# Kernel tuning notes

Measured on AMD Instinct MI355X. Metric: run time of the kernel, lower is better.

Reference implementation:

```python
import jax, jax.numpy as jnp
import numpy as np

B, C, N = 16, 256, 2048
D = C // 8  # q/k channel dim = 32
EPS = 1e-5
NEG_SLOPE = 0.2


def _conv1x1(x, w, b):
    # x: [B,C,N], w: [O,C], b: [O] -> [B,O,N]
    return jnp.einsum('oc,bcn->bon', w, x) + b[None, :, None]


def _bn(y, gamma, beta):
    # BatchNorm1d training-mode: per-channel stats over (batch, length)
    m = y.mean(axis=(0, 2), keepdims=True)
    v = y.var(axis=(0, 2), keepdims=True)  # biased, matches torch normalization
    return (y - m) * jax.lax.rsqrt(v + EPS) * gamma[None, :, None] + beta[None, :, None]


def setup_inputs() -> dict:
    key = jax.random.key(0)
    ks = jax.random.split(key, 14)
    s_qk = 1.0 / np.sqrt(C)
    return {
        'x': jax.random.normal(ks[0], (B, C, N), dtype=jnp.float32),
        'q_w': jax.random.normal(ks[1], (D, C), dtype=jnp.float32) * s_qk,
        'q_b': jnp.zeros((D,), jnp.float32),
        'q_g': jnp.ones((D,), jnp.float32),
        'q_be': jnp.zeros((D,), jnp.float32),
        'k_w': jax.random.normal(ks[2], (D, C), dtype=jnp.float32) * s_qk,
        'k_b': jnp.zeros((D,), jnp.float32),
        'k_g': jnp.ones((D,), jnp.float32),
        'k_be': jnp.zeros((D,), jnp.float32),
        'v_w': jax.random.normal(ks[3], (C, C), dtype=jnp.float32) * s_qk,
        'v_b': jnp.zeros((C,), jnp.float32),
        'v_g': jnp.ones((C,), jnp.float32),
        'v_be': jnp.zeros((C,), jnp.float32),
    }


def reference(x, q_w, q_b, q_g, q_be, k_w, k_b, k_g, k_be, v_w, v_b, v_g, v_be):
    # q, k: conv1x1 -> BN (no activation); v: conv1x1 -> BN -> LeakyReLU(0.2)
    q = _bn(_conv1x1(x, q_w, q_b), q_g, q_be)          # [B,D,N]
    k = _bn(_conv1x1(x, k_w, k_b), k_g, k_be)          # [B,D,N]
    v = jax.nn.leaky_relu(_bn(_conv1x1(x, v_w, v_b), v_g, v_be), NEG_SLOPE)  # [B,C,N]
    energy = jnp.einsum('bdn,bdm->bnm', q, k)          # [B,N,N]
    attn = jax.nn.softmax(energy, axis=-1)
    o = jnp.einsum('bcm,bnm->bcn', v, attn)            # attn applied over points
    return o + x
```

## Files before the change

kernel.cpp:

```cpp
#include <hip/hip_runtime.h>

#define BATCH 16
#define CH    256
#define NPT   2048
#define DQK   32
#define OTOT  320
#define EPSB  1e-5f
#define SLOPE 0.2f

typedef __attribute__((ext_vector_type(8))) short bf16x8;
typedef __attribute__((ext_vector_type(4))) float f32x4;

__device__ __forceinline__ unsigned short f2bf(float f) {
    unsigned u = __float_as_uint(f);
    u = (u + 0x7FFFu + ((u >> 16) & 1u)) >> 16;
    return (unsigned short)u;
}
__device__ __forceinline__ float bf2f(unsigned short h) {
    return __uint_as_float(((unsigned)h) << 16);
}
__device__ __forceinline__ unsigned cvt_pk_bf16(float a, float b) {
    unsigned r;
    asm("v_cvt_pk_bf16_f32 %0, %1, %2" : "=v"(r) : "v"(a), "v"(b));
    return r;
}

__global__ __launch_bounds__(256) void prep_kernel(
    const float* __restrict__ qw, const float* __restrict__ qb,
    const float* __restrict__ kw, const float* __restrict__ kb,
    const float* __restrict__ vw, const float* __restrict__ vb,
    unsigned short* __restrict__ Whi, unsigned short* __restrict__ Wlo,
    float* __restrict__ Bv)
{
    int idx = blockIdx.x * 256 + threadIdx.x;
    int o = idx >> 8, c = idx & 255;
    float w;
    if (o < 32)      w = qw[(size_t)o * CH + c];
    else if (o < 64) w = kw[(size_t)(o - 32) * CH + c];
    else             w = vw[(size_t)(o - 64) * CH + c];
    unsigned short wh = f2bf(w);
    float rem = w - bf2f(wh);
    Whi[idx] = wh;
    Wlo[idx] = f2bf(rem);
    if (idx < OTOT) {
        int oo = idx;
        float bb;
        if (oo < 32)      bb = qb[oo];
        else if (oo < 64) bb = kb[oo - 32];
        else              bb = vb[oo - 64];
        Bv[oo] = bb;
    }
}

__global__ __launch_bounds__(256) void conv_kernel(
    const float* __restrict__ x,
    const unsigned short* __restrict__ Whi, const unsigned short* __restrict__ Wlo,
    const float* __restrict__ Bv,
    unsigned short* __restrict__ Ybf,
    float* __restrict__ Sum, float* __restrict__ Sq)
{
    int lin = blockIdx.x;
    int vid = (lin & 7) * 160 + (lin >> 3);
    int o5  = vid % 5;
    int rem = vid / 5;
    int ob = o5 * 64;
    int n0 = (rem & 15) * 128;
    int b  = rem >> 4;

    int tid = threadIdx.x;
    int w = tid >> 6, lane = tid & 63;
    int quad = lane >> 4, l16 = lane & 15;
    int wo = w >> 1, wn = w & 1;

    __shared__ unsigned short Xh[128][40];
    __shared__ unsigned short Xl[128][40];

    int nl = tid & 127;
    int ch = tid >> 7;
    const float* xb = x + (size_t)b * CH * NPT + n0 + nl;

    f32x4 acc[2][4];
#pragma unroll
    for (int ot = 0; ot < 2; ++ot)
#pragma unroll
        for (int nt = 0; nt < 4; ++nt)
            acc[ot][nt] = (f32x4){0.f, 0.f, 0.f, 0.f};

    float xv[16];
#pragma unroll
    for (int i = 0; i < 16; ++i)
        xv[i] = xb[(size_t)(ch * 16 + i) * NPT];

    for (int ks = 0; ks < 8; ++ks) {
        __syncthreads();
#pragma unroll
        for (int g = 0; g < 4; ++g) {
            ushort4 h4, l4;
            unsigned short* ph = (unsigned short*)&h4;
            unsigned short* pl = (unsigned short*)&l4;
#pragma unroll
            for (int j = 0; j < 4; ++j) {
                float f = xv[g * 4 + j];
                unsigned short h = f2bf(f);
                ph[j] = h;
                pl[j] = f2bf(f - bf2f(h));
            }
            *(ushort4*)&Xh[nl][ch * 16 + g * 4] = h4;
            *(ushort4*)&Xl[nl][ch * 16 + g * 4] = l4;
        }
        __syncthreads();

        if (ks < 7) {
#pragma unroll
            for (int i = 0; i < 16; ++i)
                xv[i] = xb[(size_t)((ks + 1) * 32 + ch * 16 + i) * NPT];
        }

        bf16x8 ah[2], al[2];
#pragma unroll
        for (int ot = 0; ot < 2; ++ot) {
            size_t orow = (size_t)(ob + wo * 32 + ot * 16 + l16) * 256 + ks * 32 + quad * 8;
            ah[ot] = *(const bf16x8*)(Whi + orow);
            al[ot] = *(const bf16x8*)(Wlo + orow);
        }
#pragma unroll
        for (int nt = 0; nt < 4; ++nt) {
            int nr = wn * 64 + nt * 16 + l16;
            bf16x8 bh = *(const bf16x8*)&Xh[nr][quad * 8];
            bf16x8 bl = *(const bf16x8*)&Xl[nr][quad * 8];
#pragma unroll
            for (int ot = 0; ot < 2; ++ot) {
                acc[ot][nt] = __builtin_amdgcn_mfma_f32_16x16x32_bf16(ah[ot], bh, acc[ot][nt], 0, 0, 0);
                acc[ot][nt] = __builtin_amdgcn_mfma_f32_16x16x32_bf16(ah[ot], bl, acc[ot][nt], 0, 0, 0);
                acc[ot][nt] = __builtin_amdgcn_mfma_f32_16x16x32_bf16(al[ot], bh, acc[ot][nt], 0, 0, 0);
            }
        }
    }

#pragma unroll
    for (int ot = 0; ot < 2; ++ot) {
        int obase = ob + wo * 32 + ot * 16 + quad * 4;
        float bias[4], sv[4], sq[4];
#pragma unroll
        for (int r = 0; r < 4; ++r) {
            bias[r] = Bv[obase + r];
            sv[r] = 0.f; sq[r] = 0.f;
        }
#pragma unroll
        for (int nt = 0; nt < 4; ++nt) {
            int n = n0 + wn * 64 + nt * 16 + l16;
#pragma unroll
            for (int r = 0; r < 4; ++r) {
                float v = acc[ot][nt][r] + bias[r];
                Ybf[((size_t)b * OTOT + obase + r) * NPT + n] = f2bf(v);
                sv[r] += v; sq[r] += v * v;
            }
        }
#pragma unroll
        for (int r = 0; r < 4; ++r) {
            float a = sv[r], q = sq[r];
            a += __shfl_xor(a, 1); q += __shfl_xor(q, 1);
            a += __shfl_xor(a, 2); q += __shfl_xor(q, 2);
            a += __shfl_xor(a, 4); q += __shfl_xor(q, 4);
            a += __shfl_xor(a, 8); q += __shfl_xor(q, 8);
            if (l16 == 0) {
                atomicAdd(&Sum[obase + r], a);
                atomicAdd(&Sq[obase + r], q);
            }
        }
    }
}

__global__ __launch_bounds__(256) void pack_kernel(
    const unsigned short* __restrict__ Ybf,
    const float* __restrict__ Sum, const float* __restrict__ Sq,
    const float* __restrict__ qg, const float* __restrict__ qbe,
    const float* __restrict__ kg, const float* __restrict__ kbe,
    const float* __restrict__ vg, const float* __restrict__ vbe,
    unsigned short* __restrict__ QKt, unsigned short* __restrict__ Vbf)
{
    int b = blockIdx.y, n0 = blockIdx.x * 64;
    int tid = threadIdx.x;

    __shared__ float sA[OTOT], sC[OTOT];
    for (int o = tid; o < OTOT; o += 256) {
        const float inv = 1.0f / (BATCH * NPT);
        float mean = Sum[o] * inv;
        float var  = Sq[o] * inv - mean * mean;
        float g, be;
        if (o < 32)      { g = qg[o];      be = qbe[o];      }
        else if (o < 64) { g = kg[o - 32]; be = kbe[o - 32]; }
        else             { g = vg[o - 64]; be = vbe[o - 64]; }
        float a = g * rsqrtf(var + EPSB);
        sA[o] = a;
        sC[o] = be - mean * a;
    }
    __syncthreads();

    for (int e = tid; e < 4096; e += 256) {
        int c = e >> 4, n4 = (e & 15) * 4;
        ushort4 v4 = *(const ushort4*)(Ybf + ((size_t)b * OTOT + 64 + c) * NPT + n0 + n4);
        float a = sA[64 + c], cc = sC[64 + c];
        ushort4 w4;
        unsigned short* pi = (unsigned short*)&v4;
        unsigned short* po = (unsigned short*)&w4;
#pragma unroll
        for (int i = 0; i < 4; ++i) {
            float y = bf2f(pi[i]) * a + cc;
            y = (y > 0.f) ? y : SLOPE * y;
            po[i] = f2bf(y);
        }
        *(ushort4*)(Vbf + ((size_t)b * CH + c) * NPT + n0 + n4) = w4;
    }

    __shared__ unsigned short T[64][72];
    for (int e = tid; e < 1024; e += 256) {
        int o = e >> 4, n4 = (e & 15) * 4;
        ushort4 v4 = *(const ushort4*)(Ybf + ((size_t)b * OTOT + o) * NPT + n0 + n4);
        float a = sA[o], cc = sC[o];
        unsigned short* pi = (unsigned short*)&v4;
#pragma unroll
        for (int i = 0; i < 4; ++i)
            T[n4 + i][o] = f2bf(bf2f(pi[i]) * a + cc);
    }
    __syncthreads();
    for (int e = tid; e < 1024; e += 256) {
        int nn = e >> 4, o4 = (e & 15) * 4;
        ushort4 v4 = *(const ushort4*)&T[nn][o4];
        *(ushort4*)(QKt + ((size_t)b * NPT + n0 + nn) * 64 + o4) = v4;
    }
}

__global__ __launch_bounds__(256, 2) void attn_kernel(
    const unsigned short* __restrict__ QKt,
    const unsigned short* __restrict__ Vbf,
    const float* __restrict__ x,
    float* __restrict__ out)
{
    int L = blockIdx.x;
    int xcd = L & 7, k = L >> 3;
    int gi = k >> 5, n0i = k & 31;
    int b = xcd * 2 + gi;
    int n0 = n0i * 64;

    int tid = threadIdx.x;
    int w = tid >> 6, lane = tid & 63;
    int quad = lane >> 4, l16 = lane & 15;

    const unsigned short* QK = QKt + (size_t)b * NPT * 64;
    const unsigned short* V  = Vbf + (size_t)b * CH * NPT;

    __shared__ unsigned short Pbf[2][64][72];
    __shared__ float rsw[4][64];
    __shared__ float rtot[64];

    bf16x8 qa[4];
#pragma unroll
    for (int nt = 0; nt < 4; ++nt)
        qa[nt] = *(const bf16x8*)(QK + ((size_t)(n0 + nt * 16 + l16)) * 64 + quad * 8);

    f32x4 acc[4][4];
#pragma unroll
    for (int nt = 0; nt < 4; ++nt)
#pragma unroll
        for (int ct = 0; ct < 4; ++ct)
            acc[nt][ct] = (f32x4){0.f, 0.f, 0.f, 0.f};

    float rsum[4];
#pragma unroll
    for (int nt = 0; nt < 4; ++nt) rsum[nt] = 0.f;

    const f32x4 zero4 = (f32x4){0.f, 0.f, 0.f, 0.f};

    bf16x8 kb = *(const bf16x8*)(QK + ((size_t)(w * 16 + l16)) * 64 + 32 + quad * 8);

    for (int mt = 0; mt < NPT / 64; ++mt) {
        unsigned short (*Pb)[72] = Pbf[mt & 1];

        f32x4 s[4];
#pragma unroll
        for (int nt = 0; nt < 4; ++nt)
            s[nt] = __builtin_amdgcn_mfma_f32_16x16x32_bf16(kb, qa[nt], zero4, 0, 0, 0);

        if (mt < NPT / 64 - 1)
            kb = *(const bf16x8*)(QK + ((size_t)((mt + 1) * 64 + w * 16 + l16)) * 64 + 32 + quad * 8);

        bf16x8 vb[8];
#pragma unroll
        for (int u = 0; u < 8; ++u)
            vb[u] = *(const bf16x8*)(V + ((size_t)(w * 64 + (u & 3) * 16 + l16)) * NPT
                                     + mt * 64 + (u >> 2) * 32 + quad * 8);

#pragma unroll
        for (int nt = 0; nt < 4; ++nt) {
            float p0 = __expf(s[nt][0]);
            float p1 = __expf(s[nt][1]);
            float p2 = __expf(s[nt][2]);
            float p3 = __expf(s[nt][3]);
            rsum[nt] += (p0 + p1) + (p2 + p3);
            uint2 dd;
            dd.x = cvt_pk_bf16(p0, p1);
            dd.y = cvt_pk_bf16(p2, p3);
            *(uint2*)&Pb[nt * 16 + l16][w * 16 + quad * 4] = dd;
        }

        __syncthreads();

        __builtin_amdgcn_s_setprio(1);
#pragma unroll
        for (int ks = 0; ks < 2; ++ks) {
            bf16x8 pa[4];
#pragma unroll
            for (int nt = 0; nt < 4; ++nt)
                pa[nt] = *(const bf16x8*)&Pbf[mt & 1][nt * 16 + l16][ks * 32 + quad * 8];
#pragma unroll
            for (int ct = 0; ct < 4; ++ct) {
                bf16x8 vv = vb[ks * 4 + ct];
#pragma unroll
                for (int nt = 0; nt < 4; ++nt)
                    acc[nt][ct] = __builtin_amdgcn_mfma_f32_16x16x32_bf16(pa[nt], vv, acc[nt][ct], 0, 0, 0);
            }
        }
        __builtin_amdgcn_s_setprio(0);
    }

#pragma unroll
    for (int nt = 0; nt < 4; ++nt) {
        float v = rsum[nt];
        v += __shfl_xor(v, 16);
        v += __shfl_xor(v, 32);
        if (lane < 16) rsw[w][nt * 16 + lane] = v;
    }
    __syncthreads();
    if (tid < 64)
        rtot[tid] = 1.0f / (rsw[0][tid] + rsw[1][tid] + rsw[2][tid] + rsw[3][tid]);
    __syncthreads();

    float rin[4][4];
#pragma unroll
    for (int nt = 0; nt < 4; ++nt)
#pragma unroll
        for (int r = 0; r < 4; ++r) rin[nt][r] = rtot[nt * 16 + quad * 4 + r];

#pragma unroll
    for (int nt = 0; nt < 4; ++nt)
#pragma unroll
        for (int ct = 0; ct < 4; ++ct) {
            int c = w * 64 + ct * 16 + l16;
            int n = n0 + nt * 16 + quad * 4;
            size_t gi4 = ((size_t)b * CH + c) * NPT + n;
            float4 xv = *(const float4*)(x + gi4);
            float4 o;
            o.x = acc[nt][ct][0] * rin[nt][0] + xv.x;
            o.y = acc[nt][ct][1] * rin[nt][1] + xv.y;
            o.z = acc[nt][ct][2] * rin[nt][2] + xv.z;
            o.w = acc[nt][ct][3] * rin[nt][3] + xv.w;
            *(float4*)(out + gi4) = o;
        }
}

extern "C" void kernel_launch(void* const* d_in, const int* in_sizes, int n_in,
                              void* d_out, int out_size, void* d_ws, size_t ws_size,
                              hipStream_t stream)
{
    const float* x   = (const float*)d_in[0];
    const float* qw  = (const float*)d_in[1];
    const float* qb  = (const float*)d_in[2];
    const float* qg  = (const float*)d_in[3];
    const float* qbe = (const float*)d_in[4];
    const float* kw  = (const float*)d_in[5];
    const float* kb  = (const float*)d_in[6];
    const float* kg  = (const float*)d_in[7];
    const float* kbe = (const float*)d_in[8];
    const float* vw  = (const float*)d_in[9];
    const float* vb  = (const float*)d_in[10];
    const float* vg  = (const float*)d_in[11];
    const float* vbe = (const float*)d_in[12];
    float* out = (float*)d_out;

    unsigned short* Ybf = (unsigned short*)d_ws;
    unsigned short* QKt = Ybf + (size_t)BATCH * OTOT * NPT;
    unsigned short* Vbf = QKt + (size_t)BATCH * NPT * 64;
    float* tail = (float*)(Vbf + (size_t)BATCH * CH * NPT);
    float* Sum = tail;
    float* Sq  = tail + OTOT;
    unsigned short* Whi = QKt;
    unsigned short* Wlo = Whi + (size_t)CH * OTOT;
    float* Bv = (float*)(Wlo + (size_t)CH * OTOT);

    hipMemsetAsync(Sum, 0, 2 * OTOT * sizeof(float), stream);
    prep_kernel <<<320, 256, 0, stream>>>(qw, qb, kw, kb, vw, vb, Whi, Wlo, Bv);
    conv_kernel <<<1280, 256, 0, stream>>>(x, Whi, Wlo, Bv, Ybf, Sum, Sq);
    pack_kernel <<<dim3(NPT / 64, BATCH), 256, 0, stream>>>(
        Ybf, Sum, Sq, qg, qbe, kg, kbe, vg, vbe, QKt, Vbf);
    attn_kernel <<<512, 256, 0, stream>>>(QKt, Vbf, x, out);
}
```

Baseline: 260.2 us.

## Retile conv kernel so each block covers all 320 outputs for 32 points

The conv kernel now gives each block a 32-point slab of one batch with all 320 output channels, split as 80 channels per wave, instead of 64 outputs by 128 points. The whole 256-channel x slab is split into bf16 hi/lo parts and staged in shared memory once, so the per-k-step syncs and the register prefetch pipeline go away. Each x element is now read from global memory once rather than five times, one per output group. In exchange, weights are re-read by every block, and per-point stores and stat atomics are spread over more blocks with smaller point runs.

```diff
diff --git a/kernel.cpp b/kernel.cpp
--- a/kernel.cpp
+++ b/kernel.cpp
@@ -59,87 +59,70 @@
     unsigned short* __restrict__ Ybf,
     float* __restrict__ Sum, float* __restrict__ Sq)
 {
-    int lin = blockIdx.x;
-    int vid = (lin & 7) * 160 + (lin >> 3);
-    int o5  = vid % 5;
-    int rem = vid / 5;
-    int ob = o5 * 64;
-    int n0 = (rem & 15) * 128;
-    int b  = rem >> 4;
+    int b  = blockIdx.x >> 6;
+    int n0 = (blockIdx.x & 63) * 32;
 
     int tid = threadIdx.x;
     int w = tid >> 6, lane = tid & 63;
     int quad = lane >> 4, l16 = lane & 15;
-    int wo = w >> 1, wn = w & 1;
-
-    __shared__ unsigned short Xh[128][40];
-    __shared__ unsigned short Xl[128][40];
-
-    int nl = tid & 127;
-    int ch = tid >> 7;
-    const float* xb = x + (size_t)b * CH * NPT + n0 + nl;
-
-    f32x4 acc[2][4];
-#pragma unroll
-    for (int ot = 0; ot < 2; ++ot)
-#pragma unroll
-        for (int nt = 0; nt < 4; ++nt)
-            acc[ot][nt] = (f32x4){0.f, 0.f, 0.f, 0.f};
-
-    float xv[16];
-#pragma unroll
-    for (int i = 0; i < 16; ++i)
-        xv[i] = xb[(size_t)(ch * 16 + i) * NPT];
-
-    for (int ks = 0; ks < 8; ++ks) {
-        __syncthreads();
-#pragma unroll
-        for (int g = 0; g < 4; ++g) {
+
+    __shared__ unsigned short Xh[8][32][40];
+    __shared__ unsigned short Xl[8][32][40];
+
+    {
+        int sn = tid & 31;
+        int sc = tid >> 5;
+        const float* xb = x + (size_t)b * CH * NPT + n0 + sn;
+#pragma unroll
+        for (int g = 0; g < 8; ++g) {
             ushort4 h4, l4;
             unsigned short* ph = (unsigned short*)&h4;
             unsigned short* pl = (unsigned short*)&l4;
 #pragma unroll
             for (int j = 0; j < 4; ++j) {
-                float f = xv[g * 4 + j];
+                float f = xb[(size_t)(sc * 32 + g * 4 + j) * NPT];
                 unsigned short h = f2bf(f);
                 ph[j] = h;
                 pl[j] = f2bf(f - bf2f(h));
             }
-            *(ushort4*)&Xh[nl][ch * 16 + g * 4] = h4;
-            *(ushort4*)&Xl[nl][ch * 16 + g * 4] = l4;
-        }
-        __syncthreads();
-
-        if (ks < 7) {
-#pragma unroll
-            for (int i = 0; i < 16; ++i)
-                xv[i] = xb[(size_t)((ks + 1) * 32 + ch * 16 + i) * NPT];
-        }
-
-        bf16x8 ah[2], al[2];
-#pragma unroll
-        for (int ot = 0; ot < 2; ++ot) {
-            size_t orow = (size_t)(ob + wo * 32 + ot * 16 + l16) * 256 + ks * 32 + quad * 8;
-            ah[ot] = *(const bf16x8*)(Whi + orow);
-            al[ot] = *(const bf16x8*)(Wlo + orow);
-        }
-#pragma unroll
-        for (int nt = 0; nt < 4; ++nt) {
-            int nr = wn * 64 + nt * 16 + l16;
-            bf16x8 bh = *(const bf16x8*)&Xh[nr][quad * 8];
-            bf16x8 bl = *(const bf16x8*)&Xl[nr][quad * 8];
-#pragma unroll
-            for (int ot = 0; ot < 2; ++ot) {
-                acc[ot][nt] = __builtin_amdgcn_mfma_f32_16x16x32_bf16(ah[ot], bh, acc[ot][nt], 0, 0, 0);
-                acc[ot][nt] = __builtin_amdgcn_mfma_f32_16x16x32_bf16(ah[ot], bl, acc[ot][nt], 0, 0, 0);
-                acc[ot][nt] = __builtin_amdgcn_mfma_f32_16x16x32_bf16(al[ot], bh, acc[ot][nt], 0, 0, 0);
-            }
-        }
-    }
-
-#pragma unroll
-    for (int ot = 0; ot < 2; ++ot) {
-        int obase = ob + wo * 32 + ot * 16 + quad * 4;
+            *(ushort4*)&Xh[sc][sn][g * 4] = h4;
+            *(ushort4*)&Xl[sc][sn][g * 4] = l4;
+        }
+    }
+    __syncthreads();
+
+    f32x4 acc[5][2];
+#pragma unroll
+    for (int ot = 0; ot < 5; ++ot)
+#pragma unroll
+        for (int nt = 0; nt < 2; ++nt)
+            acc[ot][nt] = (f32x4){0.f, 0.f, 0.f, 0.f};
+
+#pragma unroll
+    for (int ks = 0; ks < 8; ++ks) {
+        bf16x8 bh[2], bl[2];
+#pragma unroll
+        for (int nt = 0; nt < 2; ++nt) {
+            bh[nt] = *(const bf16x8*)&Xh[ks][nt * 16 + l16][quad * 8];
+            bl[nt] = *(const bf16x8*)&Xl[ks][nt * 16 + l16][quad * 8];
+        }
+#pragma unroll
+        for (int ot = 0; ot < 5; ++ot) {
+            size_t orow = (size_t)(w * 80 + ot * 16 + l16) * 256 + ks * 32 + quad * 8;
+            bf16x8 ah = *(const bf16x8*)(Whi + orow);
+            bf16x8 al = *(const bf16x8*)(Wlo + orow);
+#pragma unroll
+            for (int nt = 0; nt < 2; ++nt) {
+                acc[ot][nt] = __builtin_amdgcn_mfma_f32_16x16x32_bf16(ah, bh[nt], acc[ot][nt], 0, 0, 0);
+                acc[ot][nt] = __builtin_amdgcn_mfma_f32_16x16x32_bf16(ah, bl[nt], acc[ot][nt], 0, 0, 0);
+                acc[ot][nt] = __builtin_amdgcn_mfma_f32_16x16x32_bf16(al, bh[nt], acc[ot][nt], 0, 0, 0);
+            }
+        }
+    }
+
+#pragma unroll
+    for (int ot = 0; ot < 5; ++ot) {
+        int obase = w * 80 + ot * 16 + quad * 4;
         float bias[4], sv[4], sq[4];
 #pragma unroll
         for (int r = 0; r < 4; ++r) {
@@ -147,8 +130,8 @@
             sv[r] = 0.f; sq[r] = 0.f;
         }
 #pragma unroll
-        for (int nt = 0; nt < 4; ++nt) {
-            int n = n0 + wn * 64 + nt * 16 + l16;
+        for (int nt = 0; nt < 2; ++nt) {
+            int n = n0 + nt * 16 + l16;
 #pragma unroll
             for (int r = 0; r < 4; ++r) {
                 float v = acc[ot][nt][r] + bias[r];
@@ -390,7 +373,7 @@
 
     hipMemsetAsync(Sum, 0, 2 * OTOT * sizeof(float), stream);
     prep_kernel <<<320, 256, 0, stream>>>(qw, qb, kw, kb, vw, vb, Whi, Wlo, Bv);
-    conv_kernel <<<1280, 256, 0, stream>>>(x, Whi, Wlo, Bv, Ybf, Sum, Sq);
+    conv_kernel <<<1024, 256, 0, stream>>>(x, Whi, Wlo, Bv, Ybf, Sum, Sq);
     pack_kernel <<<dim3(NPT / 64, BATCH), 256, 0, stream>>>(
         Ybf, Sum, Sq, qg, qbe, kg, kbe, vg, vbe, QKt, Vbf);
     attn_kernel <<<512, 256, 0, stream>>>(QKt, Vbf, x, out);
```

Measured after the change: 344.7 us. 32.5% more time.
